# Kernel optimization log

Measured on AMD Instinct MI355X. Metric: run time of the kernel, lower is better.

## Reference

```python
import jax, jax.numpy as jnp
import numpy as np

B, T, E, H = 16, 2048, 1024, 128


def setup_inputs() -> dict:
    key = jax.random.key(0)
    kx, kk, kq, kv = jax.random.split(key, 4)
    x = jax.random.normal(kx, (B, T, E), dtype=jnp.float32)
    Wk = jax.random.normal(kk, (E, H), dtype=jnp.float32) / np.sqrt(E)
    Wq = jax.random.normal(kq, (E, H), dtype=jnp.float32) / np.sqrt(E)
    Wv = jax.random.normal(kv, (E, H), dtype=jnp.float32) / np.sqrt(E)
    mask = jnp.tril(jnp.ones((T, T), dtype=jnp.int32))  # causal mask; 0 => blocked
    return {"x": x, "mask": mask, "Wk": Wk, "Wq": Wq, "Wv": Wv}


def reference(x, mask, Wk, Wq, Wv):
    # k, q, v projections (Linear without bias)
    k = x @ Wk  # [B, T, H]
    q = x @ Wq
    v = x @ Wv
    scale = 1.0 / jnp.sqrt(jnp.asarray(H, dtype=x.dtype))
    wei = jnp.einsum("bth,bsh->bts", q, k) * scale  # [B, T, T]
    neg_inf = jnp.asarray(-jnp.inf, dtype=wei.dtype)
    wei = jnp.where(mask == 0, neg_inf, wei)
    wei = jax.nn.softmax(wei, axis=-1)
    out = jnp.einsum("bts,bsh->bth", wei, v)  # [B, T, H]
    return out
```

## Files before the change

### kernel.cpp

```cpp
#include <hip/hip_runtime.h>
#include <hip/hip_bf16.h>
#include <stdint.h>

typedef __attribute__((ext_vector_type(8))) short bf16x8;
typedef __attribute__((ext_vector_type(16))) float f32x16;
typedef __attribute__((ext_vector_type(4))) float f32x4;

__device__ __forceinline__ uint32_t cvt_pk_bf16(float a, float b){
  uint32_t r;
  asm volatile("v_cvt_pk_bf16_f32 %0, %1, %2" : "=v"(r) : "v"(a), "v"(b));
  return r;
}
__device__ __forceinline__ void permswap32(uint32_t &a, uint32_t &b){
  asm volatile("v_permlane32_swap_b32 %0, %1" : "+v"(a), "+v"(b));
}
__device__ __forceinline__ unsigned short f2bf(float f){
  uint32_t u = __float_as_uint(f);
  u += 0x7fff + ((u >> 16) & 1);
  return (unsigned short)(u >> 16);
}
__device__ __forceinline__ void gload16(const void* g, void* l){
  __builtin_amdgcn_global_load_lds((const __attribute__((address_space(1))) void*)g,
                                   (__attribute__((address_space(3))) void*)l, 16, 0, 0);
}


__global__ void prep_w(const float* __restrict__ Wk, const float* __restrict__ Wq,
                       const float* __restrict__ Wv, unsigned short* __restrict__ Wt){
  int idx = blockIdx.x * 256 + threadIdx.x;
  int frag = idx >> 9;
  int r    = idx & 511;
  int ln   = r >> 3;
  int j    = r & 7;
  int kq = frag / 24;
  int nq = frag - kq * 24;
  int n  = nq * 16 + (ln & 15);
  int e  = kq * 32 + (ln >> 4) * 8 + j;
  int mat = n >> 7;
  int h   = n & 127;
  const float* src = (mat == 0) ? Wq : (mat == 1) ? Wk : Wv;
  float v = src[e * 128 + h];
  if (mat == 0) v *= (1.4426950408889634f * 0.08838834764831845f);
  Wt[idx] = f2bf(v);
}

__global__ __launch_bounds__(256, 2) void proj_gemm(
    const float* __restrict__ x, const unsigned short* __restrict__ Wt,
    unsigned short* __restrict__ Qb, unsigned short* __restrict__ Kb,
    unsigned short* __restrict__ Vt){
  __shared__ __align__(16) float          As[3][2048];
  __shared__ __align__(16) unsigned short Bs[2][12288];

  const int tid  = threadIdx.x;
  const int lane = tid & 63;
  const int w    = tid >> 6;
  const int m0   = blockIdx.x * 64;

  f32x4 acc[4][6];
  #pragma unroll
  for (int i = 0; i < 4; ++i)
    #pragma unroll
    for (int jj = 0; jj < 6; ++jj) acc[i][jj] = (f32x4){0.f, 0.f, 0.f, 0.f};

  const int lt0 = (lane >> 1), lt1 = 32 + (lane >> 1);
  const int arow0 = w * 16 + (lt0 & 15), akk0 = (lt0 >> 4) * 8 + (lane & 1) * 4;
  const int arow1 = w * 16 + (lt1 & 15), akk1 = (lt1 >> 4) * 8 + (lane & 1) * 4;
  const float* asrc0 = x + (size_t)(m0 + arow0) * 1024 + akk0;
  const float* asrc1 = x + (size_t)(m0 + arow1) * 1024 + akk1;
  const unsigned short* bsrc = Wt + (size_t)lane * 8;

  #define STAGE_A(kt, buf) {                                              \
    gload16(asrc0 + (kt) * 32, &As[buf][(2 * w + 0) * 256]);              \
    gload16(asrc1 + (kt) * 32, &As[buf][(2 * w + 1) * 256]);              \
  }
  #define STAGE_B(kt, buf) {                                              \
    _Pragma("unroll")                                                     \
    for (int jf = 0; jf < 6; ++jf){                                       \
      int f = w * 6 + jf;                                                 \
      gload16(bsrc + ((size_t)(kt) * 24 + f) * 512, &Bs[buf][f * 512]);   \
    }                                                                     \
  }

  union BU { uint32_t u[4]; bf16x8 v; };

  STAGE_B(0, 0);
  STAGE_A(0, 0);
  STAGE_A(1, 1);
  asm volatile("s_waitcnt vmcnt(2)" ::: "memory");
  __builtin_amdgcn_s_barrier();
  __builtin_amdgcn_sched_barrier(0);

  for (int ks = 0; ks < 32; ++ks){
    const int bcur = ks & 1, bnxt = bcur ^ 1;
    const int acur = ks % 3, anxt2 = (ks + 2) % 3;
    const int kb = (ks + 1 < 32) ? ks + 1 : 31;
    const int ka = (ks + 2 < 32) ? ks + 2 : 31;
    STAGE_B(kb, bnxt);
    STAGE_A(ka, anxt2);
    bf16x8 af[4];
    #pragma unroll
    for (int am = 0; am < 4; ++am){
      float4 lo = *(const float4*)&As[acur][am * 512 + lane * 8];
      float4 hi = *(const float4*)&As[acur][am * 512 + lane * 8 + 4];
      BU u; u.u[0] = cvt_pk_bf16(lo.x, lo.y); u.u[1] = cvt_pk_bf16(lo.z, lo.w);
            u.u[2] = cvt_pk_bf16(hi.x, hi.y); u.u[3] = cvt_pk_bf16(hi.z, hi.w);
      af[am] = u.v;
    }
    bf16x8 bf[6];
    #pragma unroll
    for (int bn = 0; bn < 6; ++bn)
      bf[bn] = *(const bf16x8*)&Bs[bcur][(w * 6 + bn) * 512 + lane * 8];
    __builtin_amdgcn_s_setprio(1);
    #pragma unroll
    for (int am = 0; am < 4; ++am)
      #pragma unroll
      for (int bn = 0; bn < 6; ++bn)
        acc[am][bn] = __builtin_amdgcn_mfma_f32_16x16x32_bf16(af[am], bf[bn], acc[am][bn], 0, 0, 0);
    __builtin_amdgcn_s_setprio(0);
    asm volatile("s_waitcnt vmcnt(2)" ::: "memory");
    __builtin_amdgcn_s_barrier();
    __builtin_amdgcn_sched_barrier(0);
  }

  const int b  = m0 >> 11;
  const int t0 = m0 & 2047;
  const int lr = lane & 15;
  const int lk = lane >> 4;
  #pragma unroll
  for (int am = 0; am < 4; ++am){
    #pragma unroll
    for (int bn = 0; bn < 6; ++bn){
      int c0   = w * 96 + bn * 16;
      int mat  = c0 >> 7;
      int hcol = (c0 & 127) + lr;
      int tr   = t0 + am * 16 + lk * 4;
      f32x4 v = acc[am][bn];
      if (mat <= 1){
        unsigned short* dst = (mat == 0) ? Qb : Kb;
        size_t base = (size_t)(b * 64 + (tr >> 5)) * 4096 + (size_t)(hcol >> 4) * 512 + (hcol & 15);
        #pragma unroll
        for (int jj = 0; jj < 4; ++jj)
          dst[base + (size_t)((tr + jj) & 31) * 16] = f2bf(v[jj]);
      } else {
        ushort4 pk;
        pk.x = f2bf(v[0]); pk.y = f2bf(v[1]); pk.z = f2bf(v[2]); pk.w = f2bf(v[3]);
        size_t addr = (size_t)((b * 64 + (tr >> 5)) * 4 + (hcol >> 5)) * 1024
                    + (size_t)((tr >> 4) & 1) * 512 + (size_t)(hcol & 31) * 16 + (tr & 15);
        *(ushort4*)(Vt + addr) = pk;
      }
    }
  }
  #undef STAGE_A
  #undef STAGE_B
}

__global__ __launch_bounds__(256, 2) void attn(
    const unsigned short* __restrict__ Qf, const unsigned short* __restrict__ Kf,
    const unsigned short* __restrict__ Vf, float* __restrict__ out){
  __shared__ float comb[32][132];
  __shared__ float msh[4][32];
  __shared__ float lsh[4][32];

  const int tid  = threadIdx.x;
  const int lane = tid & 63;
  const int w    = tid >> 6;
  const int bid  = blockIdx.x;
  const int xcd  = bid & 7;
  const int k    = bid >> 3;
  const int a    = k & 31;
  const int mdx  = k >> 5;
  const int b    = xcd * 2 + (mdx >> 1);
  const int c    = (mdx & 1) ? a : 63 - a;
  const int r0   = c * 32;
  const int q5   = lane & 31;
  const int hi   = lane >> 5;

  bf16x8 qf[8];
  const unsigned short* qp = Qf + (size_t)(b * 64 + c) * 4096 + q5 * 16 + hi * 8;
  #pragma unroll
  for (int f = 0; f < 8; ++f) qf[f] = *(const bf16x8*)(qp + f * 512);

  f32x16 oacc[4];
  #pragma unroll
  for (int i = 0; i < 4; ++i) oacc[i] = (f32x16)(0.f);
  float m = -1e30f, l = 0.f;

  const unsigned short* kb = Kf + (size_t)b * 64 * 4096;
  const unsigned short* vb = Vf + (size_t)b * 64 * 4096;

  bf16x8 kf[8];
  if (w <= c){
    const unsigned short* kp = kb + (size_t)w * 4096 + q5 * 16 + hi * 8;
    #pragma unroll
    for (int f = 0; f < 8; ++f) kf[f] = *(const bf16x8*)(kp + f * 512);
  }

  for (int t = w; t <= c; t += 4){
    f32x16 sacc = (f32x16)(0.f);
    #pragma unroll
    for (int f = 0; f < 8; ++f)
      sacc = __builtin_amdgcn_mfma_f32_32x32x16_bf16(kf[f], qf[f], sacc, 0, 0, 0);
    if (t + 4 <= c){
      const unsigned short* kp = kb + (size_t)(t + 4) * 4096 + q5 * 16 + hi * 8;
      #pragma unroll
      for (int f = 0; f < 8; ++f) kf[f] = *(const bf16x8*)(kp + f * 512);
    }
    bf16x8 vf[8];
    const unsigned short* vp = vb + (size_t)t * 4096 + q5 * 16 + hi * 8;
    #pragma unroll
    for (int ht = 0; ht < 4; ++ht)
      #pragma unroll
      for (int sf = 0; sf < 2; ++sf)
        vf[ht * 2 + sf] = *(const bf16x8*)(vp + ht * 1024 + sf * 512);

    float sv[16];
    #pragma unroll
    for (int r = 0; r < 16; ++r) sv[r] = sacc[r];
    if (t == c){
      #pragma unroll
      for (int r = 0; r < 16; ++r){
        int srow = (r & 3) + 8 * (r >> 2) + 4 * hi;
        if (srow > q5) sv[r] = -1e30f;
      }
    }
    float pm = sv[0];
    #pragma unroll
    for (int r = 1; r < 16; ++r) pm = fmaxf(pm, sv[r]);
    pm = fmaxf(pm, __shfl_xor(pm, 32));
    if (!__all(pm - m <= 8.0f)){
      float mn = fmaxf(m, pm);
      float al = exp2f(m - mn);
      #pragma unroll
      for (int i = 0; i < 4; ++i) oacc[i] *= al;
      l *= al;
      m = mn;
    }
    float pv[16]; float ts = 0.f;
    #pragma unroll
    for (int r = 0; r < 16; ++r){ pv[r] = exp2f(sv[r] - m); ts += pv[r]; }
    ts += __shfl_xor(ts, 32);
    l += ts;
    uint32_t w0 = cvt_pk_bf16(pv[0],  pv[1]);
    uint32_t w2 = cvt_pk_bf16(pv[4],  pv[5]);  permswap32(w0, w2);
    uint32_t w1 = cvt_pk_bf16(pv[2],  pv[3]);
    uint32_t w3 = cvt_pk_bf16(pv[6],  pv[7]);  permswap32(w1, w3);
    uint32_t w4 = cvt_pk_bf16(pv[8],  pv[9]);
    uint32_t w6 = cvt_pk_bf16(pv[12], pv[13]); permswap32(w4, w6);
    uint32_t w5 = cvt_pk_bf16(pv[10], pv[11]);
    uint32_t w7 = cvt_pk_bf16(pv[14], pv[15]); permswap32(w5, w7);
    union { uint32_t u[4]; bf16x8 v; } pf0u, pf1u;
    pf0u.u[0] = w0; pf0u.u[1] = w1; pf0u.u[2] = w2; pf0u.u[3] = w3;
    pf1u.u[0] = w4; pf1u.u[1] = w5; pf1u.u[2] = w6; pf1u.u[3] = w7;
    #pragma unroll
    for (int ht = 0; ht < 4; ++ht){
      oacc[ht] = __builtin_amdgcn_mfma_f32_32x32x16_bf16(vf[ht * 2 + 0], pf0u.v, oacc[ht], 0, 0, 0);
      oacc[ht] = __builtin_amdgcn_mfma_f32_32x32x16_bf16(vf[ht * 2 + 1], pf1u.v, oacc[ht], 0, 0, 0);
    }
  }

  if (hi == 0){ msh[w][q5] = m; lsh[w][q5] = l; }
  __syncthreads();
  {
    float mv0 = msh[0][q5], mv1 = msh[1][q5], mv2 = msh[2][q5], mv3 = msh[3][q5];
    float lv0 = lsh[0][q5], lv1 = lsh[1][q5], lv2 = lsh[2][q5], lv3 = lsh[3][q5];
    float mfm = fmaxf(fmaxf(mv0, mv1), fmaxf(mv2, mv3));
    float lf  = lv0 * exp2f(mv0 - mfm) + lv1 * exp2f(mv1 - mfm)
              + lv2 * exp2f(mv2 - mfm) + lv3 * exp2f(mv3 - mfm);
    float s = exp2f(m - mfm) / lf;
    #pragma unroll
    for (int ht = 0; ht < 4; ++ht) oacc[ht] *= s;
  }
  #pragma unroll 1
  for (int rr = 0; rr < 4; ++rr){
    if (w == rr){
      #pragma unroll
      for (int ht = 0; ht < 4; ++ht)
        #pragma unroll
        for (int r4 = 0; r4 < 4; ++r4){
          int hh = ht * 32 + 8 * r4 + 4 * hi;
          float4 add;
          add.x = oacc[ht][r4 * 4 + 0]; add.y = oacc[ht][r4 * 4 + 1];
          add.z = oacc[ht][r4 * 4 + 2]; add.w = oacc[ht][r4 * 4 + 3];
          float* p = &comb[q5][hh];
          if (rr == 0) *(float4*)p = add;
          else { float4 cur = *(const float4*)p;
                 cur.x += add.x; cur.y += add.y; cur.z += add.z; cur.w += add.w;
                 *(float4*)p = cur; }
        }
    }
    __syncthreads();
  }
  float* obase = out + ((size_t)b * 2048 + r0) * 128;
  #pragma unroll
  for (int it = 0; it < 4; ++it){
    int row = it * 8 + (tid >> 5);
    int col = (tid & 31) * 4;
    *(float4*)(obase + row * 128 + col) = *(const float4*)&comb[row][col];
  }
}

extern "C" void kernel_launch(void* const* d_in, const int* in_sizes, int n_in,
                              void* d_out, int out_size, void* d_ws, size_t ws_size,
                              hipStream_t stream){
  const float* x  = (const float*)d_in[0];
  const float* Wk = (const float*)d_in[2];
  const float* Wq = (const float*)d_in[3];
  const float* Wv = (const float*)d_in[4];
  char* ws = (char*)d_ws;
  unsigned short* Wt = (unsigned short*)(ws);
  unsigned short* Qb = (unsigned short*)(ws + (1ull  << 20));
  unsigned short* Kb = (unsigned short*)(ws + (9ull  << 20));
  unsigned short* Vt = (unsigned short*)(ws + (17ull << 20));
  float* out = (float*)d_out;

  hipLaunchKernelGGL(prep_w,    dim3(1536), dim3(256), 0, stream, Wk, Wq, Wv, Wt);
  hipLaunchKernelGGL(proj_gemm, dim3(512),  dim3(256), 0, stream, x, Wt, Qb, Kb, Vt);
  hipLaunchKernelGGL(attn,      dim3(1024), dim3(256), 0, stream, Qb, Kb, Vt, out);
}
```

Before: 89.43 us.

## Split projection GEMM columns across two blocks with simpler double-buffered staging

The projection GEMM grid doubles from 512 to 1024 blocks, and each block now computes half of the 384 output columns (192), so its accumulators and B tile shrink. The A tile is staged as separate lo/hi float buffers, and the pipeline drops from triple-buffered A with explicit vmcnt waits to a plain double buffer synchronised with __syncthreads. Launch bounds rise to 3 blocks per SM to improve occupancy and fill more CUs. In exchange, each x row tile is read twice from global memory (once per column half), and the shallower prefetch may expose more load latency.

```diff
diff --git a/kernel.cpp b/kernel.cpp
--- a/kernel.cpp
+++ b/kernel.cpp
@@ -44,83 +44,71 @@
   Wt[idx] = f2bf(v);
 }
 
-__global__ __launch_bounds__(256, 2) void proj_gemm(
+__global__ __launch_bounds__(256, 3) void proj_gemm(
     const float* __restrict__ x, const unsigned short* __restrict__ Wt,
     unsigned short* __restrict__ Qb, unsigned short* __restrict__ Kb,
     unsigned short* __restrict__ Vt){
-  __shared__ __align__(16) float          As[3][2048];
-  __shared__ __align__(16) unsigned short Bs[2][12288];
+  __shared__ __align__(16) float          Alo[2][1024];
+  __shared__ __align__(16) float          Ahi[2][1024];
+  __shared__ __align__(16) unsigned short Bs[2][6144];
 
   const int tid  = threadIdx.x;
   const int lane = tid & 63;
   const int w    = tid >> 6;
-  const int m0   = blockIdx.x * 64;
-
-  f32x4 acc[4][6];
+  const int mt   = blockIdx.x >> 1;
+  const int cb   = blockIdx.x & 1;
+  const int m0   = mt * 64;
+
+  f32x4 acc[4][3];
   #pragma unroll
   for (int i = 0; i < 4; ++i)
     #pragma unroll
-    for (int jj = 0; jj < 6; ++jj) acc[i][jj] = (f32x4){0.f, 0.f, 0.f, 0.f};
-
-  const int lt0 = (lane >> 1), lt1 = 32 + (lane >> 1);
-  const int arow0 = w * 16 + (lt0 & 15), akk0 = (lt0 >> 4) * 8 + (lane & 1) * 4;
-  const int arow1 = w * 16 + (lt1 & 15), akk1 = (lt1 >> 4) * 8 + (lane & 1) * 4;
-  const float* asrc0 = x + (size_t)(m0 + arow0) * 1024 + akk0;
-  const float* asrc1 = x + (size_t)(m0 + arow1) * 1024 + akk1;
+    for (int jj = 0; jj < 3; ++jj) acc[i][jj] = (f32x4){0.f, 0.f, 0.f, 0.f};
+
+  const float* asrc = x + (size_t)(m0 + w * 16 + (lane & 15)) * 1024 + ((lane >> 4) << 3);
   const unsigned short* bsrc = Wt + (size_t)lane * 8;
 
-  #define STAGE_A(kt, buf) {                                              \
-    gload16(asrc0 + (kt) * 32, &As[buf][(2 * w + 0) * 256]);              \
-    gload16(asrc1 + (kt) * 32, &As[buf][(2 * w + 1) * 256]);              \
-  }
-  #define STAGE_B(kt, buf) {                                              \
-    _Pragma("unroll")                                                     \
-    for (int jf = 0; jf < 6; ++jf){                                       \
-      int f = w * 6 + jf;                                                 \
-      gload16(bsrc + ((size_t)(kt) * 24 + f) * 512, &Bs[buf][f * 512]);   \
-    }                                                                     \
+  #define STAGE(kt, buf) {                                                      \
+    gload16(asrc + (kt) * 32,     &Alo[buf][w * 256]);                          \
+    gload16(asrc + (kt) * 32 + 4, &Ahi[buf][w * 256]);                          \
+    _Pragma("unroll")                                                           \
+    for (int jf = 0; jf < 3; ++jf)                                              \
+      gload16(bsrc + ((size_t)(kt) * 24 + cb * 12 + w * 3 + jf) * 512,          \
+              &Bs[buf][(w * 3 + jf) * 512]);                                    \
   }
 
   union BU { uint32_t u[4]; bf16x8 v; };
 
-  STAGE_B(0, 0);
-  STAGE_A(0, 0);
-  STAGE_A(1, 1);
-  asm volatile("s_waitcnt vmcnt(2)" ::: "memory");
-  __builtin_amdgcn_s_barrier();
-  __builtin_amdgcn_sched_barrier(0);
-
+  STAGE(0, 0);
+  __syncthreads();
+
+  #pragma unroll 2
   for (int ks = 0; ks < 32; ++ks){
-    const int bcur = ks & 1, bnxt = bcur ^ 1;
-    const int acur = ks % 3, anxt2 = (ks + 2) % 3;
-    const int kb = (ks + 1 < 32) ? ks + 1 : 31;
-    const int ka = (ks + 2 < 32) ? ks + 2 : 31;
-    STAGE_B(kb, bnxt);
-    STAGE_A(ka, anxt2);
+    const int buf = ks & 1;
+    if (ks + 1 < 32) STAGE(ks + 1, buf ^ 1);
     bf16x8 af[4];
     #pragma unroll
     for (int am = 0; am < 4; ++am){
-      float4 lo = *(const float4*)&As[acur][am * 512 + lane * 8];
-      float4 hi = *(const float4*)&As[acur][am * 512 + lane * 8 + 4];
+      float4 lo = *(const float4*)&Alo[buf][am * 256 + lane * 4];
+      float4 hi = *(const float4*)&Ahi[buf][am * 256 + lane * 4];
       BU u; u.u[0] = cvt_pk_bf16(lo.x, lo.y); u.u[1] = cvt_pk_bf16(lo.z, lo.w);
             u.u[2] = cvt_pk_bf16(hi.x, hi.y); u.u[3] = cvt_pk_bf16(hi.z, hi.w);
       af[am] = u.v;
     }
-    bf16x8 bf[6];
-    #pragma unroll
-    for (int bn = 0; bn < 6; ++bn)
-      bf[bn] = *(const bf16x8*)&Bs[bcur][(w * 6 + bn) * 512 + lane * 8];
+    bf16x8 bfr[3];
+    #pragma unroll
+    for (int bn = 0; bn < 3; ++bn)
+      bfr[bn] = *(const bf16x8*)&Bs[buf][(w * 3 + bn) * 512 + lane * 8];
     __builtin_amdgcn_s_setprio(1);
     #pragma unroll
     for (int am = 0; am < 4; ++am)
       #pragma unroll
-      for (int bn = 0; bn < 6; ++bn)
-        acc[am][bn] = __builtin_amdgcn_mfma_f32_16x16x32_bf16(af[am], bf[bn], acc[am][bn], 0, 0, 0);
+      for (int bn = 0; bn < 3; ++bn)
+        acc[am][bn] = __builtin_amdgcn_mfma_f32_16x16x32_bf16(af[am], bfr[bn], acc[am][bn], 0, 0, 0);
     __builtin_amdgcn_s_setprio(0);
-    asm volatile("s_waitcnt vmcnt(2)" ::: "memory");
-    __builtin_amdgcn_s_barrier();
-    __builtin_amdgcn_sched_barrier(0);
-  }
+    __syncthreads();
+  }
+  #undef STAGE
 
   const int b  = m0 >> 11;
   const int t0 = m0 & 2047;
@@ -129,8 +117,8 @@
   #pragma unroll
   for (int am = 0; am < 4; ++am){
     #pragma unroll
-    for (int bn = 0; bn < 6; ++bn){
-      int c0   = w * 96 + bn * 16;
+    for (int bn = 0; bn < 3; ++bn){
+      int c0   = cb * 192 + w * 48 + bn * 16;
       int mat  = c0 >> 7;
       int hcol = (c0 & 127) + lr;
       int tr   = t0 + am * 16 + lk * 4;
@@ -150,8 +138,6 @@
       }
     }
   }
-  #undef STAGE_A
-  #undef STAGE_B
 }
 
 __global__ __launch_bounds__(256, 2) void attn(
@@ -314,6 +300,6 @@
   float* out = (float*)d_out;
 
   hipLaunchKernelGGL(prep_w,    dim3(1536), dim3(256), 0, stream, Wk, Wq, Wv, Wt);
-  hipLaunchKernelGGL(proj_gemm, dim3(512),  dim3(256), 0, stream, x, Wt, Qb, Kb, Vt);
+  hipLaunchKernelGGL(proj_gemm, dim3(1024), dim3(256), 0, stream, x, Wt, Qb, Kb, Vt);
   hipLaunchKernelGGL(attn,      dim3(1024), dim3(256), 0, stream, Qb, Kb, Vt, out);
 }
```

After: 100.5 us. +12.3%, slower.

## Enlarge projection GEMM tile to 128 rows with 8 waves in 4x2 grid

Applied to the files above, without the earlier changes.

The projection GEMM now uses 512-thread blocks, each covering 128 rows of x instead of 64, with the grid halved to 256 blocks. Waves are arranged as 4 row groups by 2 column groups, each computing a 32x192 output tile. This halves how often the shared B (weight) tile is loaded per output row and changes the A staging layout. It also gives fewer blocks for 256 CUs, puts more accumulator registers on each wave, and increases LDS use.

```diff
diff --git a/kernel.cpp b/kernel.cpp
--- a/kernel.cpp
+++ b/kernel.cpp
@@ -44,41 +44,39 @@
   Wt[idx] = f2bf(v);
 }
 
-__global__ __launch_bounds__(256, 2) void proj_gemm(
+__global__ __launch_bounds__(512, 2) void proj_gemm(
     const float* __restrict__ x, const unsigned short* __restrict__ Wt,
     unsigned short* __restrict__ Qb, unsigned short* __restrict__ Kb,
     unsigned short* __restrict__ Vt){
-  __shared__ __align__(16) float          As[3][2048];
+  __shared__ __align__(16) float          As[3][4096];
   __shared__ __align__(16) unsigned short Bs[2][12288];
 
   const int tid  = threadIdx.x;
   const int lane = tid & 63;
   const int w    = tid >> 6;
-  const int m0   = blockIdx.x * 64;
-
-  f32x4 acc[4][6];
-  #pragma unroll
-  for (int i = 0; i < 4; ++i)
-    #pragma unroll
-    for (int jj = 0; jj < 6; ++jj) acc[i][jj] = (f32x4){0.f, 0.f, 0.f, 0.f};
-
-  const int lt0 = (lane >> 1), lt1 = 32 + (lane >> 1);
-  const int arow0 = w * 16 + (lt0 & 15), akk0 = (lt0 >> 4) * 8 + (lane & 1) * 4;
-  const int arow1 = w * 16 + (lt1 & 15), akk1 = (lt1 >> 4) * 8 + (lane & 1) * 4;
-  const float* asrc0 = x + (size_t)(m0 + arow0) * 1024 + akk0;
-  const float* asrc1 = x + (size_t)(m0 + arow1) * 1024 + akk1;
+  const int wr   = w >> 1;
+  const int wc   = w & 1;
+  const int m0   = blockIdx.x * 128;
+
+  f32x4 acc[2][12];
+  #pragma unroll
+  for (int i = 0; i < 2; ++i)
+    #pragma unroll
+    for (int jj = 0; jj < 12; ++jj) acc[i][jj] = (f32x4){0.f, 0.f, 0.f, 0.f};
+
+  const float* asrc = x + (size_t)(m0 + w * 16 + (lane & 15)) * 1024 + ((lane >> 4) << 3);
   const unsigned short* bsrc = Wt + (size_t)lane * 8;
 
-  #define STAGE_A(kt, buf) {                                              \
-    gload16(asrc0 + (kt) * 32, &As[buf][(2 * w + 0) * 256]);              \
-    gload16(asrc1 + (kt) * 32, &As[buf][(2 * w + 1) * 256]);              \
-  }
-  #define STAGE_B(kt, buf) {                                              \
-    _Pragma("unroll")                                                     \
-    for (int jf = 0; jf < 6; ++jf){                                       \
-      int f = w * 6 + jf;                                                 \
-      gload16(bsrc + ((size_t)(kt) * 24 + f) * 512, &Bs[buf][f * 512]);   \
-    }                                                                     \
+  #define STAGE_A(kt, buf) {                                                    \
+    gload16(asrc + (kt) * 32,     &As[buf][w * 512]);                           \
+    gload16(asrc + (kt) * 32 + 4, &As[buf][w * 512 + 256]);                     \
+  }
+  #define STAGE_B(kt, buf) {                                                    \
+    _Pragma("unroll")                                                           \
+    for (int jf = 0; jf < 3; ++jf){                                             \
+      int f = w * 3 + jf;                                                       \
+      gload16(bsrc + ((size_t)(kt) * 24 + f) * 512, &Bs[buf][f * 512]);         \
+    }                                                                           \
   }
 
   union BU { uint32_t u[4]; bf16x8 v; };
@@ -91,49 +89,49 @@
   __builtin_amdgcn_sched_barrier(0);
 
   for (int ks = 0; ks < 32; ++ks){
-    const int bcur = ks & 1, bnxt = bcur ^ 1;
-    const int acur = ks % 3, anxt2 = (ks + 2) % 3;
+    const int bcur = ks & 1;
+    const int acur = ks % 3;
     const int kb = (ks + 1 < 32) ? ks + 1 : 31;
     const int ka = (ks + 2 < 32) ? ks + 2 : 31;
-    STAGE_B(kb, bnxt);
-    STAGE_A(ka, anxt2);
-    bf16x8 af[4];
-    #pragma unroll
-    for (int am = 0; am < 4; ++am){
-      float4 lo = *(const float4*)&As[acur][am * 512 + lane * 8];
-      float4 hi = *(const float4*)&As[acur][am * 512 + lane * 8 + 4];
+    STAGE_B(kb, bcur ^ 1);
+    STAGE_A(ka, (ks + 2) % 3);
+    bf16x8 af[2];
+    #pragma unroll
+    for (int am = 0; am < 2; ++am){
+      int fr = wr * 2 + am;
+      float4 lo = *(const float4*)&As[acur][fr * 512 + lane * 4];
+      float4 hi = *(const float4*)&As[acur][fr * 512 + 256 + lane * 4];
       BU u; u.u[0] = cvt_pk_bf16(lo.x, lo.y); u.u[1] = cvt_pk_bf16(lo.z, lo.w);
             u.u[2] = cvt_pk_bf16(hi.x, hi.y); u.u[3] = cvt_pk_bf16(hi.z, hi.w);
       af[am] = u.v;
     }
-    bf16x8 bf[6];
-    #pragma unroll
-    for (int bn = 0; bn < 6; ++bn)
-      bf[bn] = *(const bf16x8*)&Bs[bcur][(w * 6 + bn) * 512 + lane * 8];
     __builtin_amdgcn_s_setprio(1);
     #pragma unroll
-    for (int am = 0; am < 4; ++am)
-      #pragma unroll
-      for (int bn = 0; bn < 6; ++bn)
-        acc[am][bn] = __builtin_amdgcn_mfma_f32_16x16x32_bf16(af[am], bf[bn], acc[am][bn], 0, 0, 0);
+    for (int bn = 0; bn < 12; ++bn){
+      bf16x8 bfr = *(const bf16x8*)&Bs[bcur][(wc * 12 + bn) * 512 + lane * 8];
+      acc[0][bn] = __builtin_amdgcn_mfma_f32_16x16x32_bf16(af[0], bfr, acc[0][bn], 0, 0, 0);
+      acc[1][bn] = __builtin_amdgcn_mfma_f32_16x16x32_bf16(af[1], bfr, acc[1][bn], 0, 0, 0);
+    }
     __builtin_amdgcn_s_setprio(0);
     asm volatile("s_waitcnt vmcnt(2)" ::: "memory");
     __builtin_amdgcn_s_barrier();
     __builtin_amdgcn_sched_barrier(0);
   }
+  #undef STAGE_A
+  #undef STAGE_B
 
   const int b  = m0 >> 11;
   const int t0 = m0 & 2047;
   const int lr = lane & 15;
   const int lk = lane >> 4;
   #pragma unroll
-  for (int am = 0; am < 4; ++am){
-    #pragma unroll
-    for (int bn = 0; bn < 6; ++bn){
-      int c0   = w * 96 + bn * 16;
+  for (int am = 0; am < 2; ++am){
+    #pragma unroll
+    for (int bn = 0; bn < 12; ++bn){
+      int c0   = wc * 192 + bn * 16;
       int mat  = c0 >> 7;
       int hcol = (c0 & 127) + lr;
-      int tr   = t0 + am * 16 + lk * 4;
+      int tr   = t0 + wr * 32 + am * 16 + lk * 4;
       f32x4 v = acc[am][bn];
       if (mat <= 1){
         unsigned short* dst = (mat == 0) ? Qb : Kb;
@@ -150,8 +148,6 @@
       }
     }
   }
-  #undef STAGE_A
-  #undef STAGE_B
 }
 
 __global__ __launch_bounds__(256, 2) void attn(
@@ -314,6 +310,6 @@
   float* out = (float*)d_out;
 
   hipLaunchKernelGGL(prep_w,    dim3(1536), dim3(256), 0, stream, Wk, Wq, Wv, Wt);
-  hipLaunchKernelGGL(proj_gemm, dim3(512),  dim3(256), 0, stream, x, Wt, Qb, Kb, Vt);
+  hipLaunchKernelGGL(proj_gemm, dim3(256),  dim3(512), 0, stream, x, Wt, Qb, Kb, Vt);
   hipLaunchKernelGGL(attn,      dim3(1024), dim3(256), 0, stream, Qb, Kb, Vt, out);
 }
```

Result: slower. 98.73 us (+10.4%).

## Replace LDS-staged pipelined projection GEMM with direct global-to-register loads

Applied to the files above, without the earlier changes.

The projection GEMM no longer stages x and the pre-packed weight fragments through a triple/double-buffered LDS pipeline using global_load_lds with barriers. Each wave now loads its A rows and B fragments straight into registers every k-step and feeds them to the MFMAs. This removes LDS traffic, barriers and waitcnt synchronisation. In exchange it loses explicit prefetch overlap, and the waves re-read x redundantly from global/L2.

```diff
diff --git a/kernel.cpp b/kernel.cpp
--- a/kernel.cpp
+++ b/kernel.cpp
@@ -18,10 +18,6 @@
   uint32_t u = __float_as_uint(f);
   u += 0x7fff + ((u >> 16) & 1);
   return (unsigned short)(u >> 16);
-}
-__device__ __forceinline__ void gload16(const void* g, void* l){
-  __builtin_amdgcn_global_load_lds((const __attribute__((address_space(1))) void*)g,
-                                   (__attribute__((address_space(3))) void*)l, 16, 0, 0);
 }
 
 
@@ -48,9 +44,6 @@
     const float* __restrict__ x, const unsigned short* __restrict__ Wt,
     unsigned short* __restrict__ Qb, unsigned short* __restrict__ Kb,
     unsigned short* __restrict__ Vt){
-  __shared__ __align__(16) float          As[3][2048];
-  __shared__ __align__(16) unsigned short Bs[2][12288];
-
   const int tid  = threadIdx.x;
   const int lane = tid & 63;
   const int w    = tid >> 6;
@@ -62,64 +55,35 @@
     #pragma unroll
     for (int jj = 0; jj < 6; ++jj) acc[i][jj] = (f32x4){0.f, 0.f, 0.f, 0.f};
 
-  const int lt0 = (lane >> 1), lt1 = 32 + (lane >> 1);
-  const int arow0 = w * 16 + (lt0 & 15), akk0 = (lt0 >> 4) * 8 + (lane & 1) * 4;
-  const int arow1 = w * 16 + (lt1 & 15), akk1 = (lt1 >> 4) * 8 + (lane & 1) * 4;
-  const float* asrc0 = x + (size_t)(m0 + arow0) * 1024 + akk0;
-  const float* asrc1 = x + (size_t)(m0 + arow1) * 1024 + akk1;
+  const float* asrc = x + (size_t)(m0 + (lane & 15)) * 1024 + ((lane >> 4) << 3);
   const unsigned short* bsrc = Wt + (size_t)lane * 8;
 
-  #define STAGE_A(kt, buf) {                                              \
-    gload16(asrc0 + (kt) * 32, &As[buf][(2 * w + 0) * 256]);              \
-    gload16(asrc1 + (kt) * 32, &As[buf][(2 * w + 1) * 256]);              \
-  }
-  #define STAGE_B(kt, buf) {                                              \
-    _Pragma("unroll")                                                     \
-    for (int jf = 0; jf < 6; ++jf){                                       \
-      int f = w * 6 + jf;                                                 \
-      gload16(bsrc + ((size_t)(kt) * 24 + f) * 512, &Bs[buf][f * 512]);   \
-    }                                                                     \
-  }
-
   union BU { uint32_t u[4]; bf16x8 v; };
 
-  STAGE_B(0, 0);
-  STAGE_A(0, 0);
-  STAGE_A(1, 1);
-  asm volatile("s_waitcnt vmcnt(2)" ::: "memory");
-  __builtin_amdgcn_s_barrier();
-  __builtin_amdgcn_sched_barrier(0);
-
   for (int ks = 0; ks < 32; ++ks){
-    const int bcur = ks & 1, bnxt = bcur ^ 1;
-    const int acur = ks % 3, anxt2 = (ks + 2) % 3;
-    const int kb = (ks + 1 < 32) ? ks + 1 : 31;
-    const int ka = (ks + 2 < 32) ? ks + 2 : 31;
-    STAGE_B(kb, bnxt);
-    STAGE_A(ka, anxt2);
+    float4 ar[8];
+    #pragma unroll
+    for (int am = 0; am < 4; ++am){
+      ar[am * 2 + 0] = *(const float4*)(asrc + am * 16384 + ks * 32);
+      ar[am * 2 + 1] = *(const float4*)(asrc + am * 16384 + ks * 32 + 4);
+    }
+    bf16x8 bfr[6];
+    #pragma unroll
+    for (int bn = 0; bn < 6; ++bn)
+      bfr[bn] = *(const bf16x8*)(bsrc + ((size_t)(ks * 24 + w * 6 + bn) << 9));
     bf16x8 af[4];
     #pragma unroll
     for (int am = 0; am < 4; ++am){
-      float4 lo = *(const float4*)&As[acur][am * 512 + lane * 8];
-      float4 hi = *(const float4*)&As[acur][am * 512 + lane * 8 + 4];
+      float4 lo = ar[am * 2 + 0], hi = ar[am * 2 + 1];
       BU u; u.u[0] = cvt_pk_bf16(lo.x, lo.y); u.u[1] = cvt_pk_bf16(lo.z, lo.w);
             u.u[2] = cvt_pk_bf16(hi.x, hi.y); u.u[3] = cvt_pk_bf16(hi.z, hi.w);
       af[am] = u.v;
     }
-    bf16x8 bf[6];
-    #pragma unroll
-    for (int bn = 0; bn < 6; ++bn)
-      bf[bn] = *(const bf16x8*)&Bs[bcur][(w * 6 + bn) * 512 + lane * 8];
-    __builtin_amdgcn_s_setprio(1);
     #pragma unroll
     for (int am = 0; am < 4; ++am)
       #pragma unroll
       for (int bn = 0; bn < 6; ++bn)
-        acc[am][bn] = __builtin_amdgcn_mfma_f32_16x16x32_bf16(af[am], bf[bn], acc[am][bn], 0, 0, 0);
-    __builtin_amdgcn_s_setprio(0);
-    asm volatile("s_waitcnt vmcnt(2)" ::: "memory");
-    __builtin_amdgcn_s_barrier();
-    __builtin_amdgcn_sched_barrier(0);
+        acc[am][bn] = __builtin_amdgcn_mfma_f32_16x16x32_bf16(af[am], bfr[bn], acc[am][bn], 0, 0, 0);
   }
 
   const int b  = m0 >> 11;
@@ -150,8 +114,6 @@
       }
     }
   }
-  #undef STAGE_A
-  #undef STAGE_B
 }
 
 __global__ __launch_bounds__(256, 2) void attn(
```

Result: slower. 119.4 us (+33.6%).
